# Performance work log

Hardware: AMD Instinct MI355X
Metric: run time of the kernel (lower is better)

Reference implementation:

```python
import jax, jax.numpy as jnp
import numpy as np
from jax import lax

U, K, POOL, STRIDE, FC = 300, 19, 7, 7, 100   # num_units, filter size, maxpool, fc_size
B, L, D = 256, 1000, 4                        # batch, seq len, DNA dim
P = (L - (K - 1) - (POOL - 1) - 1) // STRIDE + 1  # post_pool_size = 140
EPS = 1e-5  # BatchNorm eps (eval mode with running stats; Dropout is identity in eval)


def setup_inputs() -> dict:
    key = jax.random.key(0)
    ks = jax.random.split(key, 24)
    rn = lambda k, shp, s=0.1: jax.random.normal(k, shp, jnp.float32) * s
    return {
        "input_seq": jax.random.normal(ks[0], (B, L, D), jnp.float32),
        # per-unit conv (groups=U on tiled input == plain Conv1d(4, U, K))
        "w_conv": rn(ks[1], (U, D, K)), "b_conv": rn(ks[2], (U,)),
        "g1": 1.0 + rn(ks[3], (U,)), "be1": rn(ks[4], (U,)),
        "m1": rn(ks[5], (U,)), "v1": 1.0 + jax.random.uniform(ks[6], (U,), jnp.float32),
        # per-unit FC1 (grouped 1x1 conv: P -> FC per unit)
        "w_fc1": rn(ks[7], (U, FC, P)), "b_fc1": rn(ks[8], (U, FC)),
        "g2": 1.0 + rn(ks[9], (U, FC)), "be2": rn(ks[10], (U, FC)),
        "m2": rn(ks[11], (U, FC)), "v2": 1.0 + jax.random.uniform(ks[12], (U, FC), jnp.float32),
        # per-unit FC2 (grouped 1x1 conv: FC -> 1 per unit)
        "w_fc2": rn(ks[13], (U, FC)), "b_fc2": rn(ks[14], (U,)),
        "g3": 1.0 + rn(ks[15], (U,)), "be3": rn(ks[16], (U,)),
        "m3": rn(ks[17], (U,)), "v3": 1.0 + jax.random.uniform(ks[18], (U,), jnp.float32),
        # final Linear(U, 1)
        "w_out": rn(ks[19], (U, 1)), "b_out": rn(ks[20], (1,)),
    }


def reference(input_seq, w_conv, b_conv, g1, be1, m1, v1, w_fc1, b_fc1,
              g2, be2, m2, v2, w_fc2, b_fc2, g3, be3, m3, v3, w_out, b_out):
    x = jnp.transpose(input_seq, (0, 2, 1))  # B,D,L
    # grouped conv on input tiled U times: every group sees the same D=4 channels,
    # so it is exactly a plain Conv1d(D, U, K).
    conv = lax.conv_general_dilated(
        x, w_conv, (1,), 'VALID', dimension_numbers=('NCH', 'OIH', 'NCH')
    ) + b_conv[None, :, None]                 # B,U,L' (L'=L-K+1)
    a = (conv - m1[None, :, None]) * (g1 / jnp.sqrt(v1 + EPS))[None, :, None] + be1[None, :, None]
    a = jnp.exp(a)
    pooled = lax.reduce_window(a, -jnp.inf, lax.max,
                               (1, 1, POOL), (1, 1, STRIDE), 'VALID')  # B,U,P
    # Flatten->Unsqueeze->grouped 1x1 conv == per-unit matmul over P
    h = jnp.einsum('bup,ufp->buf', pooled, w_fc1) + b_fc1               # B,U,FC
    h = jax.nn.relu((h - m2) * (g2 / jnp.sqrt(v2 + EPS)) + be2)
    z = jnp.einsum('buf,uf->bu', h, w_fc2) + b_fc2                      # B,U
    z = jax.nn.relu((z - m3) * (g3 / jnp.sqrt(v3 + EPS)) + be3)
    return jax.nn.sigmoid(z @ w_out + b_out)                            # B,1
```

## Files before the change

### kernel.cpp

```cpp
#include <hip/hip_runtime.h>
#include <hip/hip_bf16.h>
#include <math.h>

#define U_   300
#define K_   19
#define FC_  100
#define B_   256
#define L_   1000
#define P_   140
#define EPS_ 1e-5f
#define WLD_ 144

typedef unsigned short ushort_t;
typedef __attribute__((ext_vector_type(8)))  short short8v;
typedef __attribute__((ext_vector_type(16))) float f32x16;

__device__ __forceinline__ ushort_t f2bf(float f) {
    union { float f; unsigned u; } a; a.f = f;
    unsigned r = a.u + 0x7fffu + ((a.u >> 16) & 1u);
    return (ushort_t)(r >> 16);
}

__global__ __launch_bounds__(256, 4)
void pack_conv_k(const float* __restrict__ w_conv, const float* __restrict__ b_conv,
                 const float* __restrict__ g1, const float* __restrict__ be1,
                 const float* __restrict__ m1, const float* __restrict__ v1,
                 ushort_t* __restrict__ w_bf, float* __restrict__ o1g)
{
    const int t = blockIdx.x * 256 + threadIdx.x;
    if (t < 320 * 80) {
        const int u = t / 80, j = t - u * 80;
        float val = 0.f;
        if (u < U_ && j < 76) {
            const int tp = j >> 2;
            const int d  = j & 3;
            const float s1 = g1[u] / sqrtf(v1[u] + EPS_);
            val = w_conv[u * 76 + 19 * d + tp] * s1;
        }
        const int nt = u >> 5, r = u & 31;
        const int kc = j >> 4, rem = j & 15;
        const int half = rem >> 3, e = rem & 7;
        w_bf[nt * 2560 + kc * 512 + half * 256 + r * 8 + e] = f2bf(val);
    }
    if (t < 320) {
        float o = 0.f;
        if (t < U_) {
            const float s1 = g1[t] / sqrtf(v1[t] + EPS_);
            o = (b_conv[t] - m1[t]) * s1 + be1[t];
        }
        o1g[t] = o;
    }
}

__global__ __launch_bounds__(448, 4)
void conv_mfma_k(const float4* __restrict__ x4,
                 const ushort_t* __restrict__ w_bf,
                 const float* __restrict__ o1g,
                 ushort_t* __restrict__ pooled)
{
    __shared__ ushort_t xls[2][880];
    __shared__ ushort_t wlds[25600];
    __shared__ float    o1l[320];
    __shared__ ushort_t stage[32][68];
    const int tid = threadIdx.x;
    const int bx  = blockIdx.x;
    const int b0  = 2 * blockIdx.y;
    const int w0  = bx * 28;
    const int l0  = w0 * 7;

    if (tid < 440) {
        const int which = (tid >= 220) ? 1 : 0;
        const int i = tid - 220 * which;
        const int gi = l0 + i;
        float4 v = make_float4(0.f, 0.f, 0.f, 0.f);
        if (gi < L_) v = x4[(size_t)(b0 + which) * L_ + gi];
        ushort4 pk4;
        pk4.x = f2bf(v.x); pk4.y = f2bf(v.y); pk4.z = f2bf(v.z); pk4.w = f2bf(v.w);
        *(ushort4*)&xls[which][4 * i] = pk4;
    }
    {
        const float4* ws = (const float4*)w_bf;
        float4* wd = (float4*)wlds;
        for (int i = tid; i < 3200; i += 448) wd[i] = ws[i];
        if (tid < 320) o1l[tid] = o1g[tid];
    }
    __syncthreads();

    const int lane = tid & 63;
    const int mt   = tid >> 6;
    const int half = lane >> 5;
    const int r32  = lane & 31;

    const int sreg = (r32 & 3) + 4 * (r32 >> 3);
    const int sh   = (r32 >> 2) & 1;
    const int off  = sreg < 7  ? sreg + 7 * sh
                   : sreg < 14 ? sreg + 7 + 7 * sh
                               : 28 + (sreg - 14) + 2 * sh;

    const char* xb0 = (const char*)&xls[0][0] + 8 * (28 * mt + off) + 16 * half;
    const char* xb1 = xb0 + 1760;
    const char* wl  = (const char*)wlds + 16 * lane;

    short8v aA0[5], aA1[5];
#pragma unroll
    for (int kc = 0; kc < 5; ++kc) {
        aA0[kc] = *(const short8v*)(xb0 + 32 * kc);
        aA1[kc] = *(const short8v*)(xb1 + 32 * kc);
    }

    const int dr  = tid / 7;
    const int dcc = tid - 7 * dr;
    const int dul = dr >> 1;
    const int dbl = dr & 1;

    const int p0off = 4 * mt + half;

    for (int nt = 0; nt < 10; ++nt) {
        short8v bfr[5];
#pragma unroll
        for (int kc = 0; kc < 5; ++kc)
            bfr[kc] = *(const short8v*)(wl + nt * 5120 + kc * 1024);
        const float o1u = o1l[nt * 32 + r32];

        f32x16 acc0 = {};
        f32x16 acc1 = {};
#pragma unroll
        for (int kc = 0; kc < 5; ++kc) {
            acc0 = __builtin_amdgcn_mfma_f32_32x32x16_bf16(aA0[kc], bfr[kc], acc0, 0, 0, 0);
            acc1 = __builtin_amdgcn_mfma_f32_32x32x16_bf16(aA1[kc], bfr[kc], acc1, 0, 0, 0);
        }

        float m00 = acc0[0], m01 = acc0[7];
        float m10 = acc1[0], m11 = acc1[7];
#pragma unroll
        for (int j = 1; j < 7; ++j)  { m00 = fmaxf(m00, acc0[j]); m10 = fmaxf(m10, acc1[j]); }
#pragma unroll
        for (int j = 8; j < 14; ++j) { m01 = fmaxf(m01, acc0[j]); m11 = fmaxf(m11, acc1[j]); }

        stage[r32][p0off]          = f2bf(__expf(m00 + o1u));
        stage[r32][p0off + 2]      = f2bf(__expf(m01 + o1u));
        stage[r32][32 + p0off]     = f2bf(__expf(m10 + o1u));
        stage[r32][32 + p0off + 2] = f2bf(__expf(m11 + o1u));
        __syncthreads();

        const int ug = nt * 32 + dul;
        if (ug < U_) {
            const ushort4 st = *(const ushort4*)&stage[dul][dbl * 32 + 4 * dcc];
            *(ushort4*)&pooled[((size_t)ug * B_ + (b0 + dbl)) * P_ + w0 + 4 * dcc] = st;
        }
        __syncthreads();
    }
}

__global__ __launch_bounds__(256, 3)
void fc_mfma_k(const ushort_t* __restrict__ pooled,
               const float* __restrict__ w_fc1,
               const float* __restrict__ b_fc1,
               const float* __restrict__ g2,
               const float* __restrict__ be2,
               const float* __restrict__ m2,
               const float* __restrict__ v2,
               const float* __restrict__ w_fc2,
               const float* __restrict__ b_fc2,
               const float* __restrict__ g3,
               const float* __restrict__ be3,
               const float* __restrict__ m3,
               const float* __restrict__ v3,
               float* __restrict__ zT)
{
    __shared__ ushort_t wlds[FC_ * WLD_];
    __shared__ float zred[128][33];
    const int tid  = threadIdx.x;
    const int bid = blockIdx.x;
    int u, bt;
    if (bid < 592) {
        const int r = bid & 7, k = bid >> 3;
        bt = k & 1;
        u  = (k >> 1) * 8 + r;
    } else {
        const int t = bid - 592;
        u  = 296 + (t >> 1);
        bt = t & 1;
    }

    const float* __restrict__ wsrc = w_fc1 + (size_t)u * FC_ * P_;
    for (int idx = tid; idx < FC_ * 35; idx += 256) {
        const int f = idx / 35, j = idx - f * 35;
        const float4 v = *(const float4*)(wsrc + f * P_ + 4 * j);
        ushort4 pk;
        pk.x = f2bf(v.x); pk.y = f2bf(v.y); pk.z = f2bf(v.z); pk.w = f2bf(v.w);
        *(ushort4*)&wlds[f * WLD_ + 4 * j] = pk;
    }
    for (int idx = tid; idx < FC_ * 4; idx += 256) {
        const int f = idx >> 2, k = 140 + (idx & 3);
        wlds[f * WLD_ + k] = 0;
    }
    __syncthreads();

    const int lane = tid & 63;
    const int wv   = tid >> 6;
    const int half = lane >> 5;
    const int r32  = lane & 31;

    const int brow = bt * 128 + wv * 32 + r32;
    const ushort_t* __restrict__ abase =
        pooled + ((size_t)u * B_ + brow) * P_ + half * 8;

    const ushort_t* __restrict__ bl0 = &wlds[r32 * WLD_ + half * 8];
    const ushort_t* __restrict__ bl1 = &wlds[(32 + r32) * WLD_ + half * 8];
    const ushort_t* __restrict__ bl2 = &wlds[(64 + r32) * WLD_ + half * 8];
    const int f3c = (96 + r32 < FC_) ? (96 + r32) : (FC_ - 1);
    const ushort_t* __restrict__ bl3 = &wlds[f3c * WLD_ + half * 8];

    short8v ac = *(const short8v*)(abase);
    f32x16 acc0 = {}, acc1 = {}, acc2 = {}, acc3 = {};
#pragma unroll
    for (int kc = 0; kc < 9; ++kc) {
        const int kn = (kc < 8) ? kc + 1 : kc;
        const short8v an = *(const short8v*)(abase + kn * 16);
        const short8v b0 = *(const short8v*)(bl0 + kc * 16);
        const short8v b1 = *(const short8v*)(bl1 + kc * 16);
        const short8v b2 = *(const short8v*)(bl2 + kc * 16);
        const short8v b3 = *(const short8v*)(bl3 + kc * 16);
        acc0 = __builtin_amdgcn_mfma_f32_32x32x16_bf16(ac, b0, acc0, 0, 0, 0);
        acc1 = __builtin_amdgcn_mfma_f32_32x32x16_bf16(ac, b1, acc1, 0, 0, 0);
        acc2 = __builtin_amdgcn_mfma_f32_32x32x16_bf16(ac, b2, acc2, 0, 0, 0);
        acc3 = __builtin_amdgcn_mfma_f32_32x32x16_bf16(ac, b3, acc3, 0, 0, 0);
        ac = an;
    }

    float s2[4], o2[4], w2[4];
#pragma unroll
    for (int n = 0; n < 4; ++n) {
        const int f = n * 32 + r32;
        if (f < FC_) {
            const int fg = u * FC_ + f;
            const float ss = g2[fg] / sqrtf(v2[fg] + EPS_);
            s2[n] = ss;
            o2[n] = (b_fc1[fg] - m2[fg]) * ss + be2[fg];
            w2[n] = w_fc2[fg];
        } else {
            s2[n] = 0.f; o2[n] = 0.f; w2[n] = 0.f;
        }
    }
#pragma unroll
    for (int rg = 0; rg < 16; ++rg) {
        const int row = (rg & 3) + 8 * (rg >> 2) + 4 * half;
        float s = fmaxf(fmaf(acc0[rg], s2[0], o2[0]), 0.f) * w2[0];
        s = fmaf(fmaxf(fmaf(acc1[rg], s2[1], o2[1]), 0.f), w2[1], s);
        s = fmaf(fmaxf(fmaf(acc2[rg], s2[2], o2[2]), 0.f), w2[2], s);
        s = fmaf(fmaxf(fmaf(acc3[rg], s2[3], o2[3]), 0.f), w2[3], s);
        zred[wv * 32 + row][r32] = s;
    }
    __syncthreads();

    if (tid < 128) {
        float s = 0.f;
#pragma unroll
        for (int j = 0; j < 32; ++j) s += zred[tid][j];
        const float s3 = g3[u] / sqrtf(v3[u] + EPS_);
        const float o3 = (b_fc2[u] - m3[u]) * s3 + be3[u];
        zT[(size_t)(bt * 128 + tid) * 304 + u] = fmaxf(fmaf(s, s3, o3), 0.f);
    }
}

__global__ __launch_bounds__(64, 8)
void out_k(const float* __restrict__ zT,
           const float* __restrict__ w_out,
           const float* __restrict__ b_out,
           float* __restrict__ out)
{
    const int lane = threadIdx.x;
    const int b    = blockIdx.x;
    const float4* zr = (const float4*)(zT + (size_t)b * 304);
    const float4* w4 = (const float4*)w_out;

    float s = 0.f;
    for (int i = lane; i < 75; i += 64) {
        const float4 z = zr[i], w = w4[i];
        s += z.x * w.x + z.y * w.y + z.z * w.z + z.w * w.w;
    }
#pragma unroll
    for (int o = 32; o > 0; o >>= 1) s += __shfl_xor(s, o);
    if (lane == 0)
        out[b] = 1.0f / (1.0f + __expf(-(s + b_out[0])));
}

extern "C" void kernel_launch(void* const* d_in, const int* in_sizes, int n_in,
                              void* d_out, int out_size, void* d_ws, size_t ws_size,
                              hipStream_t stream)
{
    const float* input_seq = (const float*)d_in[0];
    const float* w_conv    = (const float*)d_in[1];
    const float* b_conv    = (const float*)d_in[2];
    const float* g1        = (const float*)d_in[3];
    const float* be1       = (const float*)d_in[4];
    const float* m1        = (const float*)d_in[5];
    const float* v1        = (const float*)d_in[6];
    const float* w_fc1     = (const float*)d_in[7];
    const float* b_fc1     = (const float*)d_in[8];
    const float* g2        = (const float*)d_in[9];
    const float* be2       = (const float*)d_in[10];
    const float* m2        = (const float*)d_in[11];
    const float* v2        = (const float*)d_in[12];
    const float* w_fc2     = (const float*)d_in[13];
    const float* b_fc2     = (const float*)d_in[14];
    const float* g3        = (const float*)d_in[15];
    const float* be3       = (const float*)d_in[16];
    const float* m3        = (const float*)d_in[17];
    const float* v3        = (const float*)d_in[18];
    const float* w_out     = (const float*)d_in[19];
    const float* b_out     = (const float*)d_in[20];

    char* p = (char*)d_ws;
    ushort_t* pooled = (ushort_t*)p;   p += (size_t)B_ * U_ * P_ * 2;
    ushort_t* w_bf   = (ushort_t*)p;   p += 320 * 80 * 2;
    float*    o1g    = (float*)p;      p += 320 * 4;
    float*    zT     = (float*)p;      p += (size_t)B_ * 304 * 4;

    pack_conv_k<<<dim3(100), 256, 0, stream>>>(
        w_conv, b_conv, g1, be1, m1, v1, w_bf, o1g);

    conv_mfma_k<<<dim3(5, 128), 448, 0, stream>>>(
        (const float4*)input_seq, w_bf, o1g, pooled);

    fc_mfma_k<<<dim3(600), 256, 0, stream>>>(
        pooled, w_fc1, b_fc1, g2, be2, m2, v2, w_fc2, b_fc2,
        g3, be3, m3, v3, zT);

    out_k<<<dim3(B_), 64, 0, stream>>>(zT, w_out, b_out, (float*)d_out);
}
```

Before: 55.78 us.

## Process one batch per conv block and stage all units before a single store pass

The conv kernel now handles one batch element per block instead of two, doubling the grid along y. It stages pooled outputs for all 10 unit tiles in a larger LDS buffer and writes them to global memory in one pass after a single barrier. This removes the two barriers per unit tile. In exchange it halves reuse of the LDS-loaded weights per block (each block still loads the full weight table) and uses more shared memory for staging, which may reduce occupancy.

```diff
diff --git a/kernel.cpp b/kernel.cpp
--- a/kernel.cpp
+++ b/kernel.cpp
@@ -58,25 +58,23 @@
                  const float* __restrict__ o1g,
                  ushort_t* __restrict__ pooled)
 {
-    __shared__ ushort_t xls[2][880];
+    __shared__ ushort_t xls[880];
     __shared__ ushort_t wlds[25600];
     __shared__ float    o1l[320];
-    __shared__ ushort_t stage[32][68];
+    __shared__ ushort_t stage[320][30];
     const int tid = threadIdx.x;
     const int bx  = blockIdx.x;
-    const int b0  = 2 * blockIdx.y;
+    const int b   = blockIdx.y;
     const int w0  = bx * 28;
     const int l0  = w0 * 7;
 
-    if (tid < 440) {
-        const int which = (tid >= 220) ? 1 : 0;
-        const int i = tid - 220 * which;
-        const int gi = l0 + i;
+    if (tid < 220) {
+        const int gi = l0 + tid;
         float4 v = make_float4(0.f, 0.f, 0.f, 0.f);
-        if (gi < L_) v = x4[(size_t)(b0 + which) * L_ + gi];
+        if (gi < L_) v = x4[(size_t)b * L_ + gi];
         ushort4 pk4;
         pk4.x = f2bf(v.x); pk4.y = f2bf(v.y); pk4.z = f2bf(v.z); pk4.w = f2bf(v.w);
-        *(ushort4*)&xls[which][4 * i] = pk4;
+        *(ushort4*)&xls[4 * tid] = pk4;
     }
     {
         const float4* ws = (const float4*)w_bf;
@@ -97,24 +95,17 @@
                    : sreg < 14 ? sreg + 7 + 7 * sh
                                : 28 + (sreg - 14) + 2 * sh;
 
-    const char* xb0 = (const char*)&xls[0][0] + 8 * (28 * mt + off) + 16 * half;
-    const char* xb1 = xb0 + 1760;
-    const char* wl  = (const char*)wlds + 16 * lane;
-
-    short8v aA0[5], aA1[5];
-#pragma unroll
-    for (int kc = 0; kc < 5; ++kc) {
-        aA0[kc] = *(const short8v*)(xb0 + 32 * kc);
-        aA1[kc] = *(const short8v*)(xb1 + 32 * kc);
-    }
-
-    const int dr  = tid / 7;
-    const int dcc = tid - 7 * dr;
-    const int dul = dr >> 1;
-    const int dbl = dr & 1;
-
-    const int p0off = 4 * mt + half;
-
+    const char* xb = (const char*)xls + 8 * (28 * mt + off) + 16 * half;
+    const char* wl = (const char*)wlds + 16 * lane;
+
+    short8v aA[5];
+#pragma unroll
+    for (int kc = 0; kc < 5; ++kc)
+        aA[kc] = *(const short8v*)(xb + 32 * kc);
+
+    const int pcol = 4 * mt + half;
+
+#pragma unroll
     for (int nt = 0; nt < 10; ++nt) {
         short8v bfr[5];
 #pragma unroll
@@ -122,33 +113,31 @@
             bfr[kc] = *(const short8v*)(wl + nt * 5120 + kc * 1024);
         const float o1u = o1l[nt * 32 + r32];
 
-        f32x16 acc0 = {};
-        f32x16 acc1 = {};
-#pragma unroll
-        for (int kc = 0; kc < 5; ++kc) {
-            acc0 = __builtin_amdgcn_mfma_f32_32x32x16_bf16(aA0[kc], bfr[kc], acc0, 0, 0, 0);
-            acc1 = __builtin_amdgcn_mfma_f32_32x32x16_bf16(aA1[kc], bfr[kc], acc1, 0, 0, 0);
+        f32x16 acc = {};
+#pragma unroll
+        for (int kc = 0; kc < 5; ++kc)
+            acc = __builtin_amdgcn_mfma_f32_32x32x16_bf16(aA[kc], bfr[kc], acc, 0, 0, 0);
+
+        float m0 = acc[0], m1 = acc[7];
+#pragma unroll
+        for (int j = 1; j < 7; ++j)  m0 = fmaxf(m0, acc[j]);
+#pragma unroll
+        for (int j = 8; j < 14; ++j) m1 = fmaxf(m1, acc[j]);
+
+        stage[nt * 32 + r32][pcol]     = f2bf(__expf(m0 + o1u));
+        stage[nt * 32 + r32][pcol + 2] = f2bf(__expf(m1 + o1u));
+    }
+    __syncthreads();
+
+#pragma unroll
+    for (int i = 0; i < 5; ++i) {
+        const int idx = tid + 448 * i;
+        const int row = idx / 7;
+        const int cc  = idx - 7 * row;
+        if (row < U_) {
+            const ushort4 st = *(const ushort4*)&stage[row][4 * cc];
+            *(ushort4*)&pooled[((size_t)row * B_ + b) * P_ + w0 + 4 * cc] = st;
         }
-
-        float m00 = acc0[0], m01 = acc0[7];
-        float m10 = acc1[0], m11 = acc1[7];
-#pragma unroll
-        for (int j = 1; j < 7; ++j)  { m00 = fmaxf(m00, acc0[j]); m10 = fmaxf(m10, acc1[j]); }
-#pragma unroll
-        for (int j = 8; j < 14; ++j) { m01 = fmaxf(m01, acc0[j]); m11 = fmaxf(m11, acc1[j]); }
-
-        stage[r32][p0off]          = f2bf(__expf(m00 + o1u));
-        stage[r32][p0off + 2]      = f2bf(__expf(m01 + o1u));
-        stage[r32][32 + p0off]     = f2bf(__expf(m10 + o1u));
-        stage[r32][32 + p0off + 2] = f2bf(__expf(m11 + o1u));
-        __syncthreads();
-
-        const int ug = nt * 32 + dul;
-        if (ug < U_) {
-            const ushort4 st = *(const ushort4*)&stage[dul][dbl * 32 + 4 * dcc];
-            *(ushort4*)&pooled[((size_t)ug * B_ + (b0 + dbl)) * P_ + w0 + 4 * dcc] = st;
-        }
-        __syncthreads();
     }
 }
 
@@ -321,7 +310,7 @@
     pack_conv_k<<<dim3(100), 256, 0, stream>>>(
         w_conv, b_conv, g1, be1, m1, v1, w_bf, o1g);
 
-    conv_mfma_k<<<dim3(5, 128), 448, 0, stream>>>(
+    conv_mfma_k<<<dim3(5, B_), 448, 0, stream>>>(
         (const float4*)input_seq, w_bf, o1g, pooled);
 
     fc_mfma_k<<<dim3(600), 256, 0, stream>>>(
```

Result: no change. 55.10 us (-1.2%).
